# Kernel tuning notes

Measured on AMD Instinct MI355X. Metric: run time of the kernel, lower is better.

The kernel has to match this reference:

```python
import jax, jax.numpy as jnp
import numpy as np

BN_EPS = 1e-5


def setup_inputs() -> dict:
    key = jax.random.key(0)
    ks = jax.random.split(key, 6)
    N, C, T, V = 64, 64, 300, 25
    num_A, O = 3, 64
    x = jax.random.normal(ks[0], (N, C, T, V), dtype=jnp.float32)
    A = jax.random.uniform(ks[1], (num_A, V, V), dtype=jnp.float32)
    # 1x1 conv weights per adjacency branch: W[a, o, c], bias b[a, o]
    W = jax.random.normal(ks[2], (num_A, O, C), dtype=jnp.float32) * (1.0 / np.sqrt(C))
    b = jax.random.normal(ks[3], (num_A, O), dtype=jnp.float32) * 0.01
    gamma = jnp.ones((O,), dtype=jnp.float32)
    beta = jnp.zeros((O,), dtype=jnp.float32)
    return {"x": x, "A": A, "W": W, "b": b, "gamma": gamma, "beta": beta}


def reference(x, A, W, b, gamma, beta):
    # x: [N, C, T, V]; A: [num_A, V, V]; W: [num_A, O, C]; b: [num_A, O]
    # For each branch a: xa = x @ A_a over the joint dim V, then a 1x1 conv
    # (channel mix W_a + bias b_a), accumulated over branches.
    z = jnp.einsum('nctv,avw->anctw', x, A)          # [num_A, N, C, T, V]
    y = jnp.einsum('anctw,aoc->notw', z, W)          # [N, O, T, V]
    y = y + jnp.sum(b, axis=0)[None, :, None, None]
    # BatchNorm2d (training mode: batch statistics over N, T, V per channel)
    mean = jnp.mean(y, axis=(0, 2, 3), keepdims=True)
    var = jnp.mean((y - mean) ** 2, axis=(0, 2, 3), keepdims=True)
    y = (y - mean) * jax.lax.rsqrt(var + BN_EPS)
    y = y * gamma[None, :, None, None] + beta[None, :, None, None]
    return jax.nn.relu(y)
```

## Files before the change

kernel.cpp:

```cpp
#include <hip/hip_runtime.h>


typedef __attribute__((ext_vector_type(8))) short short8;
typedef __attribute__((ext_vector_type(4))) float f32x4;

static __device__ __forceinline__ float bf2f(unsigned short u) {
    return __uint_as_float(((unsigned)u) << 16);
}
static __device__ __forceinline__ unsigned short f2bf(float f) {
    unsigned u = __float_as_uint(f);
    u += 0x7FFFu + ((u >> 16) & 1u);
    return (unsigned short)(u >> 16);
}
static __device__ __forceinline__ unsigned pack2bf(float a, float b) {
    return (unsigned)f2bf(a) | ((unsigned)f2bf(b) << 16);
}

#define MFMA16(a, b, c) __builtin_amdgcn_mfma_f32_16x16x32_bf16((a), (b), (c), 0, 0, 0)

#define ZSTRIDE 72
#define NSLOT   64
#define XTOT    30720000u

union U16x8 { uint4 q; unsigned u[4]; short8 s; unsigned short h[8]; };

__global__ __launch_bounds__(256, 5)
void gcn_k1(const void* __restrict__ xg, const void* __restrict__ Ag,
            const void* __restrict__ Wg, const void* __restrict__ gammag,
            float* __restrict__ pslots, unsigned short* __restrict__ y_ws)
{
    const int tid  = threadIdx.x;
    const int wv   = tid >> 6;
    const int lane = tid & 63;
    const int n16  = lane & 15;
    const int kg   = lane >> 4;
    const int bx   = blockIdx.x;
    const int nb   = bx / 75;
    const int tile = bx - nb * 75;
    const int t    = tile * 4 + wv;

    const bool isbf = (*(const unsigned*)gammag) == 0x3F803F80u;

    __shared__ __align__(16) unsigned short zsT[112 * ZSTRIDE];
    __shared__ __align__(16) unsigned short AsT[3 * 4 * 32 * 8];
    __shared__ float red[128];

    if (tid < 128) red[tid] = 0.f;
    for (int s = tid; s < 432; s += 256)
        ((unsigned*)(zsT + 100 * ZSTRIDE))[s] = 0;

    short8 wfrag[3][2];
    #pragma unroll
    for (int a = 0; a < 3; ++a)
        #pragma unroll
        for (int k2 = 0; k2 < 2; ++k2) {
            const int off = (a * 64 + wv * 16 + n16) * 64 + k2 * 32 + kg * 8;
            if (isbf) {
                wfrag[a][k2] = *(const short8*)((const unsigned short*)Wg + off);
            } else {
                const float* wp = (const float*)Wg + off;
                const float4 w0 = *(const float4*)wp;
                const float4 w1 = *(const float4*)(wp + 4);
                U16x8 f;
                f.u[0] = pack2bf(w0.x, w0.y); f.u[1] = pack2bf(w0.z, w0.w);
                f.u[2] = pack2bf(w1.x, w1.y); f.u[3] = pack2bf(w1.z, w1.w);
                wfrag[a][k2] = f.s;
            }
        }

    for (int s = tid; s < 3072; s += 256) {
        const int a = s >> 10, w = (s >> 5) & 31, v = s & 31;
        unsigned short val = 0;
        if (v < 25 && w < 25) {
            const int src = (a * 25 + v) * 25 + w;
            val = isbf ? ((const unsigned short*)Ag)[src] : f2bf(((const float*)Ag)[src]);
        }
        AsT[((a * 4 + (v >> 3)) * 32 + w) * 8 + (v & 7)] = val;
    }

    short8 af[4];
    if (isbf) {
        const unsigned short* xb = (const unsigned short*)xg;
        #pragma unroll
        for (int mt = 0; mt < 4; ++mt) {
            const unsigned base = ((unsigned)(nb * 64 + mt * 16 + n16) * 300u
                                   + (unsigned)t) * 25u + (unsigned)(kg * 8);
            U16x8 r;
            if (base + 8u > XTOT) {
                r.q = make_uint4(0, 0, 0, 0);
                r.h[0] = xb[base];
            } else if ((t & 1) == 0) {
                const unsigned* p = (const unsigned*)(xb + base);
                r.u[0] = p[0]; r.u[1] = p[1]; r.u[2] = p[2]; r.u[3] = p[3];
            } else {
                const unsigned* p = (const unsigned*)(xb + base - 1);
                const unsigned tail = xb[base + 7];
                r.u[0] = (p[0] >> 16) | (p[1] << 16);
                r.u[1] = (p[1] >> 16) | (p[2] << 16);
                r.u[2] = (p[2] >> 16) | (p[3] << 16);
                r.u[3] = (p[3] >> 16) | (tail    << 16);
            }
            af[mt] = r.s;
        }
    } else {
        const float* xf = (const float*)xg;
        #pragma unroll
        for (int mt = 0; mt < 4; ++mt) {
            const unsigned base = ((unsigned)(nb * 64 + mt * 16 + n16) * 300u
                                   + (unsigned)t) * 25u + (unsigned)(kg * 8);
            U16x8 r;
            if (base + 8u > XTOT) {
                r.q = make_uint4(0, 0, 0, 0);
                r.h[0] = f2bf(xf[base]);
            } else {
                float f[8];
                #pragma unroll
                for (int j = 0; j < 8; ++j) f[j] = xf[base + j];
                r.u[0] = pack2bf(f[0], f[1]); r.u[1] = pack2bf(f[2], f[3]);
                r.u[2] = pack2bf(f[4], f[5]); r.u[3] = pack2bf(f[6], f[7]);
            }
            af[mt] = r.s;
        }
    }

    __syncthreads();

    f32x4 acc[7];
    const f32x4 zero4 = (f32x4){0.f, 0.f, 0.f, 0.f};
    #pragma unroll
    for (int mt = 0; mt < 7; ++mt) acc[mt] = zero4;

    #pragma unroll
    for (int a = 0; a < 3; ++a) {
        const short8 bA0 = *(const short8*)&AsT[((a * 4 + kg) * 32 +      n16) * 8];
        const short8 bA1 = *(const short8*)&AsT[((a * 4 + kg) * 32 + 16 + n16) * 8];
        #pragma unroll
        for (int mt = 0; mt < 4; ++mt) {
            const f32x4 d0 = MFMA16(af[mt], bA0, zero4);
            const f32x4 d1 = MFMA16(af[mt], bA1, zero4);
            const int h = mt * 16 + kg * 4;
            *(uint2*)&zsT[(wv * 25 + n16) * ZSTRIDE + h] =
                make_uint2(pack2bf(d0[0], d0[1]), pack2bf(d0[2], d0[3]));
            if (n16 < 9)
                *(uint2*)&zsT[(wv * 25 + 16 + n16) * ZSTRIDE + h] =
                    make_uint2(pack2bf(d1[0], d1[1]), pack2bf(d1[2], d1[3]));
        }
        __syncthreads();

        #pragma unroll
        for (int mt = 0; mt < 7; ++mt) {
            #pragma unroll
            for (int k2 = 0; k2 < 2; ++k2) {
                const short8 bf = *(const short8*)&zsT[(mt * 16 + n16) * ZSTRIDE
                                                       + k2 * 32 + kg * 8];
                acc[mt] = MFMA16(wfrag[a][k2], bf, acc[mt]);
            }
        }
        if (a < 2) __syncthreads();
    }

    #pragma unroll
    for (int r = 0; r < 4; ++r) {
        const int o = 16 * wv + kg * 4 + r;
        const unsigned rowbase = (unsigned)(nb * 64 + o) * 7500u + (unsigned)tile * 100u;
        float s = 0.f, q = 0.f;
        #pragma unroll
        for (int mt = 0; mt < 7; ++mt) {
            const float v = acc[mt][r];
            const bool valid = (mt < 6) | (n16 < 4);
            const float vm = valid ? v : 0.f;
            s += vm; q += vm * vm;
            const float vhi = __shfl_xor(v, 1);
            if (((n16 & 1) == 0) && valid)
                *(unsigned*)(y_ws + rowbase + (unsigned)(mt * 16 + n16)) = pack2bf(v, vhi);
        }
        #pragma unroll
        for (int off = 1; off < 16; off <<= 1) {
            s += __shfl_xor(s, off);
            q += __shfl_xor(q, off);
        }
        if (n16 == 0) { atomicAdd(&red[o], s); atomicAdd(&red[64 + o], q); }
    }

    __syncthreads();
    if (tid < 128) atomicAdd(&pslots[(bx & (NSLOT - 1)) * 128 + tid], red[tid]);
}

__global__ __launch_bounds__(128)
void gcn_kred(const float* __restrict__ pslots, float* __restrict__ gfin)
{
    const int t = threadIdx.x;
    float s = 0.f;
    #pragma unroll
    for (int sl = 0; sl < NSLOT; ++sl)
        s += pslots[sl * 128 + t];
    gfin[t] = s;
}

__global__ __launch_bounds__(256)
void gcn_k2(const float* __restrict__ gfin, const unsigned* __restrict__ y32,
            const void* __restrict__ gammag, const void* __restrict__ betag,
            void* __restrict__ outg)
{
    __shared__ float sc[64], sh[64];
    const int tid = threadIdx.x;
    const bool isbf = (*(const unsigned*)gammag) == 0x3F803F80u;

    if (tid < 64) {
        const float inv  = 1.0f / 480000.0f;
        const float mean = gfin[tid] * inv;
        const float var  = gfin[64 + tid] * inv - mean * mean;
        const float rstd = rsqrtf(var + 1e-5f);
        float g, be;
        if (isbf) { g = bf2f(((const unsigned short*)gammag)[tid]); be = bf2f(((const unsigned short*)betag)[tid]); }
        else      { g = ((const float*)gammag)[tid];                be = ((const float*)betag)[tid]; }
        sc[tid] = g * rstd;
        sh[tid] = be - mean * g * rstd;
    }
    __syncthreads();

    const unsigned i = blockIdx.x * 256u + (unsigned)tid;
    const uint4 u = ((const uint4*)y32)[i];
    const unsigned b = i * 4u;
    unsigned wv[4] = {u.x, u.y, u.z, u.w};
    float res[8];
    #pragma unroll
    for (int j = 0; j < 4; ++j) {
        const unsigned o = ((b + j) / 3750u) & 63u;
        const float scl = sc[o], shf = sh[o];
        const float v0 = bf2f((unsigned short)(wv[j] & 0xFFFFu));
        const float v1 = bf2f((unsigned short)(wv[j] >> 16));
        res[2 * j]     = fmaxf(fmaf(v0, scl, shf), 0.f);
        res[2 * j + 1] = fmaxf(fmaf(v1, scl, shf), 0.f);
    }
    if (isbf) {
        uint4 outp;
        outp.x = pack2bf(res[0], res[1]);
        outp.y = pack2bf(res[2], res[3]);
        outp.z = pack2bf(res[4], res[5]);
        outp.w = pack2bf(res[6], res[7]);
        ((uint4*)outg)[i] = outp;
    } else {
        float4 f0 = make_float4(res[0], res[1], res[2], res[3]);
        float4 f1 = make_float4(res[4], res[5], res[6], res[7]);
        ((float4*)outg)[2 * i]     = f0;
        ((float4*)outg)[2 * i + 1] = f1;
    }
}

extern "C" void kernel_launch(void* const* d_in, const int* in_sizes, int n_in,
                              void* d_out, int out_size, void* d_ws, size_t ws_size,
                              hipStream_t stream)
{
    (void)in_sizes; (void)n_in; (void)out_size; (void)ws_size;
    const void* x     = d_in[0];
    const void* A     = d_in[1];
    const void* W     = d_in[2];
    const void* gamma = d_in[4];
    const void* beta  = d_in[5];

    float*          pslots = (float*)d_ws;
    float*          gfin   = (float*)((char*)d_ws + 32768);
    unsigned short* y_ws   = (unsigned short*)((char*)d_ws + 33280);

    hipMemsetAsync(d_ws, 0, 32768, stream);
    gcn_k1<<<dim3(64 * 75), dim3(256), 0, stream>>>(x, A, W, gamma, pslots, y_ws);
    gcn_kred<<<dim3(1), dim3(128), 0, stream>>>(pslots, gfin);
    gcn_k2<<<dim3(15000), dim3(256), 0, stream>>>(gfin, (const unsigned*)y_ws, gamma, beta, d_out);
}
```

Before: 332.9 us.

## Make each wave compute all output channels for its own timestep, removing block barriers

Each wave now owns a private LDS slice and computes all 64 output channels for its single timestep instead of 16 channels across all four waves' timesteps. This removes the per-branch __syncthreads between the adjacency stage and the channel-mix stage, replacing them with lgkmcnt waits. W fragments are now reloaded from global memory inside the loop rather than kept in registers. The y stores become 16-bit scattered writes instead of packed 32-bit writes. The tradeoff is more global W traffic and narrower stores in exchange for fewer block-wide synchronisations.

```diff
diff --git a/kernel.cpp b/kernel.cpp
--- a/kernel.cpp
+++ b/kernel.cpp
@@ -18,9 +18,9 @@
 
 #define MFMA16(a, b, c) __builtin_amdgcn_mfma_f32_16x16x32_bf16((a), (b), (c), 0, 0, 0)
 
-#define ZSTRIDE 72
-#define NSLOT   64
-#define XTOT    30720000u
+#define ZSTR  72
+#define NSLOT 64
+#define XTOT  30720000u
 
 union U16x8 { uint4 q; unsigned u[4]; short8 s; unsigned short h[8]; };
 
@@ -41,32 +41,11 @@
 
     const bool isbf = (*(const unsigned*)gammag) == 0x3F803F80u;
 
-    __shared__ __align__(16) unsigned short zsT[112 * ZSTRIDE];
+    __shared__ __align__(16) unsigned short zs[4][32 * ZSTR];
     __shared__ __align__(16) unsigned short AsT[3 * 4 * 32 * 8];
     __shared__ float red[128];
 
     if (tid < 128) red[tid] = 0.f;
-    for (int s = tid; s < 432; s += 256)
-        ((unsigned*)(zsT + 100 * ZSTRIDE))[s] = 0;
-
-    short8 wfrag[3][2];
-    #pragma unroll
-    for (int a = 0; a < 3; ++a)
-        #pragma unroll
-        for (int k2 = 0; k2 < 2; ++k2) {
-            const int off = (a * 64 + wv * 16 + n16) * 64 + k2 * 32 + kg * 8;
-            if (isbf) {
-                wfrag[a][k2] = *(const short8*)((const unsigned short*)Wg + off);
-            } else {
-                const float* wp = (const float*)Wg + off;
-                const float4 w0 = *(const float4*)wp;
-                const float4 w1 = *(const float4*)(wp + 4);
-                U16x8 f;
-                f.u[0] = pack2bf(w0.x, w0.y); f.u[1] = pack2bf(w0.z, w0.w);
-                f.u[2] = pack2bf(w1.x, w1.y); f.u[3] = pack2bf(w1.z, w1.w);
-                wfrag[a][k2] = f.s;
-            }
-        }
 
     for (int s = tid; s < 3072; s += 256) {
         const int a = s >> 10, w = (s >> 5) & 31, v = s & 31;
@@ -125,13 +104,18 @@
 
     __syncthreads();
 
-    f32x4 acc[7];
+    unsigned short* const zw = &zs[wv][0];
     const f32x4 zero4 = (f32x4){0.f, 0.f, 0.f, 0.f};
-    #pragma unroll
-    for (int mt = 0; mt < 7; ++mt) acc[mt] = zero4;
-
-    #pragma unroll
+    f32x4 acc[4][2];
+    #pragma unroll
+    for (int mtp = 0; mtp < 4; ++mtp)
+        #pragma unroll
+        for (int nt = 0; nt < 2; ++nt) acc[mtp][nt] = zero4;
+
     for (int a = 0; a < 3; ++a) {
+        asm volatile("s_waitcnt lgkmcnt(0)" ::: "memory");
+        __builtin_amdgcn_sched_barrier(0);
+
         const short8 bA0 = *(const short8*)&AsT[((a * 4 + kg) * 32 +      n16) * 8];
         const short8 bA1 = *(const short8*)&AsT[((a * 4 + kg) * 32 + 16 + n16) * 8];
         #pragma unroll
@@ -139,47 +123,70 @@
             const f32x4 d0 = MFMA16(af[mt], bA0, zero4);
             const f32x4 d1 = MFMA16(af[mt], bA1, zero4);
             const int h = mt * 16 + kg * 4;
-            *(uint2*)&zsT[(wv * 25 + n16) * ZSTRIDE + h] =
+            *(uint2*)&zw[n16 * ZSTR + h] =
                 make_uint2(pack2bf(d0[0], d0[1]), pack2bf(d0[2], d0[3]));
             if (n16 < 9)
-                *(uint2*)&zsT[(wv * 25 + 16 + n16) * ZSTRIDE + h] =
+                *(uint2*)&zw[(16 + n16) * ZSTR + h] =
                     make_uint2(pack2bf(d1[0], d1[1]), pack2bf(d1[2], d1[3]));
         }
-        __syncthreads();
-
-        #pragma unroll
-        for (int mt = 0; mt < 7; ++mt) {
+
+        asm volatile("s_waitcnt lgkmcnt(0)" ::: "memory");
+        __builtin_amdgcn_sched_barrier(0);
+
+        short8 bf[2][2];
+        #pragma unroll
+        for (int nt = 0; nt < 2; ++nt)
+            #pragma unroll
+            for (int k2 = 0; k2 < 2; ++k2)
+                bf[nt][k2] = *(const short8*)&zw[(nt * 16 + n16) * ZSTR
+                                                 + k2 * 32 + kg * 8];
+
+        #pragma unroll
+        for (int mtp = 0; mtp < 4; ++mtp) {
+            short8 wf[2];
             #pragma unroll
             for (int k2 = 0; k2 < 2; ++k2) {
-                const short8 bf = *(const short8*)&zsT[(mt * 16 + n16) * ZSTRIDE
-                                                       + k2 * 32 + kg * 8];
-                acc[mt] = MFMA16(wfrag[a][k2], bf, acc[mt]);
-            }
-        }
-        if (a < 2) __syncthreads();
-    }
-
-    #pragma unroll
-    for (int r = 0; r < 4; ++r) {
-        const int o = 16 * wv + kg * 4 + r;
-        const unsigned rowbase = (unsigned)(nb * 64 + o) * 7500u + (unsigned)tile * 100u;
-        float s = 0.f, q = 0.f;
-        #pragma unroll
-        for (int mt = 0; mt < 7; ++mt) {
-            const float v = acc[mt][r];
-            const bool valid = (mt < 6) | (n16 < 4);
-            const float vm = valid ? v : 0.f;
-            s += vm; q += vm * vm;
-            const float vhi = __shfl_xor(v, 1);
-            if (((n16 & 1) == 0) && valid)
-                *(unsigned*)(y_ws + rowbase + (unsigned)(mt * 16 + n16)) = pack2bf(v, vhi);
-        }
-        #pragma unroll
-        for (int off = 1; off < 16; off <<= 1) {
-            s += __shfl_xor(s, off);
-            q += __shfl_xor(q, off);
-        }
-        if (n16 == 0) { atomicAdd(&red[o], s); atomicAdd(&red[64 + o], q); }
+                const int off = (a * 64 + mtp * 16 + n16) * 64 + k2 * 32 + kg * 8;
+                if (isbf) {
+                    wf[k2] = *(const short8*)((const unsigned short*)Wg + off);
+                } else {
+                    const float* wp = (const float*)Wg + off;
+                    const float4 w0 = *(const float4*)wp;
+                    const float4 w1 = *(const float4*)(wp + 4);
+                    U16x8 f;
+                    f.u[0] = pack2bf(w0.x, w0.y); f.u[1] = pack2bf(w0.z, w0.w);
+                    f.u[2] = pack2bf(w1.x, w1.y); f.u[3] = pack2bf(w1.z, w1.w);
+                    wf[k2] = f.s;
+                }
+            }
+            #pragma unroll
+            for (int nt = 0; nt < 2; ++nt)
+                #pragma unroll
+                for (int k2 = 0; k2 < 2; ++k2)
+                    acc[mtp][nt] = MFMA16(wf[k2], bf[nt][k2], acc[mtp][nt]);
+        }
+    }
+
+    #pragma unroll
+    for (int mtp = 0; mtp < 4; ++mtp) {
+        #pragma unroll
+        for (int r = 0; r < 4; ++r) {
+            const int o = mtp * 16 + kg * 4 + r;
+            const unsigned rowbase =
+                ((unsigned)(nb * 64 + o) * 300u + (unsigned)t) * 25u;
+            const float v0 = acc[mtp][0][r];
+            const float v1 = acc[mtp][1][r];
+            y_ws[rowbase + n16] = f2bf(v0);
+            if (n16 < 9) y_ws[rowbase + 16 + n16] = f2bf(v1);
+            float s = v0 + (n16 < 9 ? v1 : 0.f);
+            float q = v0 * v0 + (n16 < 9 ? v1 * v1 : 0.f);
+            #pragma unroll
+            for (int off = 1; off < 16; off <<= 1) {
+                s += __shfl_xor(s, off);
+                q += __shfl_xor(q, off);
+            }
+            if (n16 == 0) { atomicAdd(&red[o], s); atomicAdd(&red[64 + o], q); }
+        }
     }
 
     __syncthreads();
```

Result: slower. 396.1 us (+19.0%).
